# Optimization experiments

Measured on AMD Instinct MI355X. Metric: run time of the kernel, lower is better.

## Reference

```python
import jax, jax.numpy as jnp
import numpy as np

EPS = 1e-5

def _ln(x, g, b):
    m = jnp.mean(x, axis=-1, keepdims=True)
    v = jnp.mean((x - m) ** 2, axis=-1, keepdims=True)
    return (x - m) * jax.lax.rsqrt(v + EPS) * g + b


def setup_inputs() -> dict:
    key = jax.random.key(0)
    B, T, C, H, A = 4, 1024, 1024, 16, 64
    ks = jax.random.split(key, 16)
    s = 0.02
    inp = {
        "x": jax.random.normal(ks[0], (B, T, C), jnp.float32),
        "ln1_g": jnp.ones((C,), jnp.float32), "ln1_b": jnp.zeros((C,), jnp.float32),
        "ln2_g": jnp.ones((C,), jnp.float32), "ln2_b": jnp.zeros((C,), jnp.float32),
        "ln3_g": jnp.ones((C,), jnp.float32), "ln3_b": jnp.zeros((C,), jnp.float32),
        "wq": jax.random.normal(ks[1], (C, C), jnp.float32) * s, "bq": jnp.zeros((C,), jnp.float32),
        "wk": jax.random.normal(ks[2], (C, C), jnp.float32) * s, "bk": jnp.zeros((C,), jnp.float32),
        "wv": jax.random.normal(ks[3], (C, C), jnp.float32) * s, "bv": jnp.zeros((C,), jnp.float32),
        "wo": jax.random.normal(ks[4], (C, C), jnp.float32) * s, "bo": jnp.zeros((C,), jnp.float32),
        "w1": jax.random.normal(ks[5], (C, 4 * C), jnp.float32) * s, "b1": jnp.zeros((4 * C,), jnp.float32),
        "w2": jax.random.normal(ks[6], (4 * C, C), jnp.float32) * s, "b2": jnp.zeros((C,), jnp.float32),
        "wd": jax.random.normal(ks[7], (C, A), jnp.float32) * 1e-4, "bd": jnp.zeros((A,), jnp.float32),
        "wu": jax.random.normal(ks[8], (A, C), jnp.float32) * 1e-4, "bu": jnp.zeros((C,), jnp.float32),
    }
    return inp


def _block(x, ln1_g, ln1_b, ln2_g, ln2_b, ln3_g, ln3_b,
           wq, bq, wk, bk, wv, bv, wo, bo, w1, b1, w2, b2, wd, bd, wu, bu):
    B, T, C = x.shape
    H = 16
    D = C // H
    normed = _ln(x, ln3_g, ln3_b)  # ln3 of original input, used by adapter

    # --- causal self-attention on ln1(x) ---
    h = _ln(x, ln1_g, ln1_b)
    q = (h @ wq + bq).reshape(B, T, H, D)
    k = (h @ wk + bk).reshape(B, T, H, D)
    v = (h @ wv + bv).reshape(B, T, H, D)
    att = jnp.einsum('bqhd,bkhd->bhqk', q, k) * (1.0 / np.sqrt(D))
    causal = jnp.tril(jnp.ones((T, T), bool))
    att = jnp.where(causal, att, -jnp.inf)
    att = jax.nn.softmax(att, axis=-1)
    y = jnp.einsum('bhqk,bkhd->bqhd', att, v).reshape(B, T, C)
    attn_out = y @ wo + bo

    hidden = x + attn_out
    # --- MLP on ln2(hidden) ---
    m = _ln(hidden, ln2_g, ln2_b)
    mlp_out = jax.nn.gelu(m @ w1 + b1, approximate=False) @ w2 + b2
    forward_states = hidden + mlp_out

    # --- adapter on ln3(original x) ---
    a = jax.nn.relu(normed @ wd + bd) @ wu + bu

    # dropout is identity (p=0 / eval)
    return hidden + forward_states + a


def reference(x, ln1_g, ln1_b, ln2_g, ln2_b, ln3_g, ln3_b,
              wq, bq, wk, bk, wv, bv, wo, bo, w1, b1, w2, b2, wd, bd, wu, bu):
    return _block(x, ln1_g, ln1_b, ln2_g, ln2_b, ln3_g, ln3_b,
                  wq, bq, wk, bk, wv, bv, wo, bo, w1, b1, w2, b2, wd, bd, wu, bu)
```

## Files before the change

### kernel.cpp

```cpp
#include <hip/hip_runtime.h>

typedef unsigned short u16;
typedef __bf16 bf16x8 __attribute__((ext_vector_type(8)));
typedef u16    u16x8  __attribute__((ext_vector_type(8)));
typedef float  f32x4  __attribute__((ext_vector_type(4)));

__device__ __forceinline__ u16 f2bf(float f) {
    union { float f; unsigned u; } x{f};
    unsigned r = x.u + 0x7fffu + ((x.u >> 16) & 1u);
    return (u16)(r >> 16);
}

__device__ __forceinline__ f32x4 mfma16(bf16x8 a, bf16x8 b, f32x4 c) {
    return __builtin_amdgcn_mfma_f32_16x16x32_bf16(a, b, c, 0, 0, 0);
}

__device__ __forceinline__ void async_ld16(const void* g, void* l) {
    __builtin_amdgcn_global_load_lds(
        (const __attribute__((address_space(1))) unsigned int*)g,
        (__attribute__((address_space(3))) unsigned int*)l, 16, 0, 0);
}

__global__ void transpose_to_bf16(const float* __restrict__ in, u16* __restrict__ out,
                                  int K, int N) {
    __shared__ float tile[64][65];
    const int k0 = blockIdx.y * 64, n0 = blockIdx.x * 64;
    const int tid = threadIdx.x;
    const int rr = tid >> 4, cc = tid & 15;
#pragma unroll
    for (int it = 0; it < 4; ++it) {
        const int r = rr + it * 16;
        float4 v = *(const float4*)(in + (long)(k0 + r) * N + n0 + cc * 4);
        tile[r][cc * 4 + 0] = v.x; tile[r][cc * 4 + 1] = v.y;
        tile[r][cc * 4 + 2] = v.z; tile[r][cc * 4 + 3] = v.w;
    }
    __syncthreads();
#pragma unroll
    for (int it = 0; it < 4; ++it) {
        const int n = rr + it * 16;
        ushort4 o;
        o.x = f2bf(tile[cc * 4 + 0][n]);
        o.y = f2bf(tile[cc * 4 + 1][n]);
        o.z = f2bf(tile[cc * 4 + 2][n]);
        o.w = f2bf(tile[cc * 4 + 3][n]);
        *(ushort4*)(out + (long)(n0 + n) * K + k0 + cc * 4) = o;
    }
}

__global__ void concat_bias(const float* __restrict__ bq, const float* __restrict__ bk,
                            const float* __restrict__ bv, float* __restrict__ out) {
    int i = blockIdx.x * 256 + threadIdx.x;
    out[i] = i < 1024 ? bq[i] : (i < 2048 ? bk[i - 1024] : bv[i - 2048]);
}

__global__ void ln_dual_kernel(const float* __restrict__ x,
                               const float* __restrict__ g1, const float* __restrict__ b1,
                               const float* __restrict__ g3, const float* __restrict__ b3,
                               u16* __restrict__ out1, u16* __restrict__ out3) {
    const int row = blockIdx.x;
    const long base = (long)row * 1024;
    const int t = threadIdx.x;
    float4 v = ((const float4*)(x + base))[t];
    float s = v.x + v.y + v.z + v.w;
    float ss = v.x * v.x + v.y * v.y + v.z * v.z + v.w * v.w;
    for (int o = 32; o > 0; o >>= 1) { s += __shfl_down(s, o); ss += __shfl_down(ss, o); }
    __shared__ float red[8];
    if ((t & 63) == 0) { red[t >> 6] = s; red[(t >> 6) + 4] = ss; }
    __syncthreads();
    float sum = red[0] + red[1] + red[2] + red[3];
    float sq  = red[4] + red[5] + red[6] + red[7];
    const float mean = sum * (1.f / 1024.f);
    const float rstd = rsqrtf(sq * (1.f / 1024.f) - mean * mean + 1e-5f);
    float4 G1 = ((const float4*)g1)[t], B1 = ((const float4*)b1)[t];
    float4 G3 = ((const float4*)g3)[t], B3 = ((const float4*)b3)[t];
    float n0 = (v.x - mean) * rstd, n1 = (v.y - mean) * rstd;
    float n2 = (v.z - mean) * rstd, n3 = (v.w - mean) * rstd;
    ushort4 o1, o3;
    o1.x = f2bf(n0 * G1.x + B1.x); o1.y = f2bf(n1 * G1.y + B1.y);
    o1.z = f2bf(n2 * G1.z + B1.z); o1.w = f2bf(n3 * G1.w + B1.w);
    o3.x = f2bf(n0 * G3.x + B3.x); o3.y = f2bf(n1 * G3.y + B3.y);
    o3.z = f2bf(n2 * G3.z + B3.z); o3.w = f2bf(n3 * G3.w + B3.w);
    ((ushort4*)(out1 + base))[t] = o1;
    ((ushort4*)(out3 + base))[t] = o3;
}

__global__ void ln_single_kernel(const float* __restrict__ x,
                                 const float* __restrict__ g, const float* __restrict__ b,
                                 u16* __restrict__ out) {
    const int row = blockIdx.x;
    const long base = (long)row * 1024;
    const int t = threadIdx.x;
    float4 v = ((const float4*)(x + base))[t];
    float s = v.x + v.y + v.z + v.w;
    float ss = v.x * v.x + v.y * v.y + v.z * v.z + v.w * v.w;
    for (int o = 32; o > 0; o >>= 1) { s += __shfl_down(s, o); ss += __shfl_down(ss, o); }
    __shared__ float red[8];
    if ((t & 63) == 0) { red[t >> 6] = s; red[(t >> 6) + 4] = ss; }
    __syncthreads();
    float sum = red[0] + red[1] + red[2] + red[3];
    float sq  = red[4] + red[5] + red[6] + red[7];
    const float mean = sum * (1.f / 1024.f);
    const float rstd = rsqrtf(sq * (1.f / 1024.f) - mean * mean + 1e-5f);
    float4 G = ((const float4*)g)[t], B = ((const float4*)b)[t];
    ushort4 o;
    o.x = f2bf((v.x - mean) * rstd * G.x + B.x);
    o.y = f2bf((v.y - mean) * rstd * G.y + B.y);
    o.z = f2bf((v.z - mean) * rstd * G.z + B.z);
    o.w = f2bf((v.w - mean) * rstd * G.w + B.w);
    ((ushort4*)(out + base))[t] = o;
}

__global__ void transpose_v(const u16* __restrict__ qkv, u16* __restrict__ vT) {
    const int bh = blockIdx.z, b = bh >> 4, hh = bh & 15;
    const int t0 = blockIdx.x * 32, d0 = blockIdx.y * 32;
    __shared__ u16 tile[32][33];
    const u16* src = qkv + (long)(b * 1024) * 3072 + 2048 + hh * 64;
    for (int i = threadIdx.y; i < 32; i += 8)
        tile[i][threadIdx.x] = src[(long)(t0 + i) * 3072 + d0 + threadIdx.x];
    __syncthreads();
    u16* dst = vT + (long)bh * 64 * 1024;
    for (int i = threadIdx.y; i < 32; i += 8)
        dst[(long)(d0 + i) * 1024 + t0 + threadIdx.x] = tile[threadIdx.x][i];
}

template <int BN, typename Epi>
__global__ __launch_bounds__(256, 2)
void gemm_kernel(const u16* __restrict__ A, const u16* __restrict__ Bt,
                 int M, int N, int K, Epi epi) {
    constexpr int AE = 128 * 32;
    constexpr int BE = BN * 32;
    constexpr int MI = (BN == 128) ? 4 : 2;
    __shared__ u16 sm[4][AE + BE];
    const int tid = threadIdx.x;
    const int m0 = blockIdx.y * 128;
    const int n0 = blockIdx.x * BN;
    const int wid = tid >> 6, lane = tid & 63;
    const int lr = lane & 15, lh = lane >> 4;
    const int wm = (BN == 128) ? (wid >> 1) * 64 : wid * 32;
    const int wn = (BN == 128) ? (wid & 1) * 64 : 0;

    const int cr = lane >> 2, lq = lane & 3;
    const int ra0 = wid * 32 + cr, ra1 = ra0 + 16;
    const int qa0 = lq ^ (ra0 & 3) ^ ((ra0 >> 2) & 3);
    const int qa1 = lq ^ (ra1 & 3) ^ ((ra1 >> 2) & 3);
    const long aoff0 = (long)(m0 + ra0) * K + qa0 * 8;
    const long aoff1 = (long)(m0 + ra1) * K + qa1 * 8;
    const int la0 = wid * 1024, la1 = la0 + 512;

    long boff0, boff1 = 0;
    int lb0, lb1 = 0;
    if (BN == 128) {
        boff0 = (long)min(n0 + ra0, N - 1) * K + qa0 * 8;
        boff1 = (long)min(n0 + ra1, N - 1) * K + qa1 * 8;
        lb0 = AE + wid * 1024; lb1 = lb0 + 512;
    } else {
        const int rb = wid * 16 + cr;
        const int qb = lq ^ (rb & 3) ^ ((rb >> 2) & 3);
        boff0 = (long)min(n0 + rb, N - 1) * K + qb * 8;
        lb0 = AE + wid * 512;
    }

    const int qoff = ((lh ^ (lr & 3) ^ ((lr >> 2) & 3)) & 3) * 8;

    f32x4 acc[MI][4] = {};
    const int nk = K / 32;

    auto stage = [&](int kt) {
        const long ko = (long)kt * 32;
        u16* s = sm[kt & 3];
        async_ld16(A + aoff0 + ko, s + la0);
        async_ld16(A + aoff1 + ko, s + la1);
        async_ld16(Bt + boff0 + ko, s + lb0);
        if constexpr (BN == 128) async_ld16(Bt + boff1 + ko, s + lb1);
    };
    auto compute = [&](int kt) {
        const u16* sA = sm[kt & 3];
        const u16* sB = sA + AE;
        bf16x8 af[MI], bfr[4];
#pragma unroll
        for (int i = 0; i < MI; ++i)
            af[i] = *(const bf16x8*)(sA + (wm + i * 16 + lr) * 32 + qoff);
#pragma unroll
        for (int j = 0; j < 4; ++j)
            bfr[j] = *(const bf16x8*)(sB + (wn + j * 16 + lr) * 32 + qoff);
#pragma unroll
        for (int i = 0; i < MI; ++i)
#pragma unroll
            for (int j = 0; j < 4; ++j)
                acc[i][j] = mfma16(af[i], bfr[j], acc[i][j]);
    };

    stage(0);
    stage(1);
    __syncthreads();
    for (int kt = 0; kt < nk; kt += 2) {
        if (kt + 2 < nk) stage(kt + 2);
        if (kt + 3 < nk) stage(kt + 3);
        compute(kt);
        compute(kt + 1);
        __syncthreads();
    }

#pragma unroll
    for (int i = 0; i < MI; ++i)
#pragma unroll
        for (int j = 0; j < 4; ++j) {
            const int col = n0 + wn + j * 16 + lr;
            if (col < N) {
#pragma unroll
                for (int r = 0; r < 4; ++r) {
                    const int row = m0 + wm + i * 16 + lh * 4 + r;
                    epi(row, col, acc[i][j][r]);
                }
            }
        }
}

struct EpiBF16Bias {
    u16* out; const float* bias; int ldo;
    __device__ void operator()(int r, int c, float v) const {
        out[(long)r * ldo + c] = f2bf(v + bias[c]);
    }
};
struct EpiResid {
    float* hidden; const float* bias; const float* x;
    __device__ void operator()(int r, int c, float v) const {
        long i = (long)r * 1024 + c; hidden[i] = v + bias[c] + x[i];
    }
};
struct EpiGelu {
    u16* out; const float* bias;
    __device__ void operator()(int r, int c, float v) const {
        float x = v + bias[c];
        float g = 0.5f * x * (1.f + erff(x * 0.70710678118654752f));
        out[(long)r * 4096 + c] = f2bf(g);
    }
};
struct EpiReluBF16 {
    u16* out; const float* bias;
    __device__ void operator()(int r, int c, float v) const {
        out[(long)r * 64 + c] = f2bf(fmaxf(v + bias[c], 0.f));
    }
};
struct EpiAdapter {
    float* out; const float* bias; const float* hidden;
    __device__ void operator()(int r, int c, float v) const {
        long i = (long)r * 1024 + c; out[i] = 2.f * hidden[i] + v + bias[c];
    }
};
struct EpiAddOut {
    float* out; const float* bias;
    __device__ void operator()(int r, int c, float v) const {
        long i = (long)r * 1024 + c; out[i] += v + bias[c];
    }
};

__global__ __launch_bounds__(256, 2)
void attn_kernel(const u16* __restrict__ qkv, const u16* __restrict__ vT,
                 u16* __restrict__ y) {
    const int bh = blockIdx.x, b = bh >> 4, hh = bh & 15;
    const int q0 = blockIdx.y * 128;
    const int tid = threadIdx.x, wid = tid >> 6, lane = tid & 63;
    const int lr = lane & 15, lh = lane >> 4;
    const int qw = q0 + wid * 32;

    __shared__ u16 smK[64 * 72];
    __shared__ u16 smV[64 * 72];
    __shared__ u16 smP[4 * 32 * 72];
    u16* pw = smP + wid * (32 * 72);

    const u16* qbase = qkv + (long)(b * 1024) * 3072 + hh * 64;
    const u16* kbase = qbase + 1024;
    const u16* vbase = vT + (long)bh * 64 * 1024;

    bf16x8 a_q[2][2];
#pragma unroll
    for (int mt = 0; mt < 2; ++mt)
#pragma unroll
        for (int ks = 0; ks < 2; ++ks) {
            uint4 t = *(const uint4*)(qbase + (long)(qw + mt * 16 + lr) * 3072 + ks * 32 + lh * 8);
            a_q[mt][ks] = __builtin_bit_cast(bf16x8, t);
        }

    bf16x8 ones;
    { u16x8 t = {0x3F80, 0x3F80, 0x3F80, 0x3F80, 0x3F80, 0x3F80, 0x3F80, 0x3F80};
      ones = __builtin_bit_cast(bf16x8, t); }

    f32x4 o_acc[2][4] = {};
    f32x4 l_acc[2] = {};
    f32x4 m_run[2] = {{-1e30f, -1e30f, -1e30f, -1e30f}, {-1e30f, -1e30f, -1e30f, -1e30f}};

    const int ntiles = q0 / 64 + 2;
    const int ck = tid >> 3, cs = (tid & 7) * 8;
    const int ck2 = (tid + 256) >> 3, cs2 = ((tid + 256) & 7) * 8;
    for (int kt = 0; kt < ntiles; ++kt) {
        const int k0 = kt * 64;
        __syncthreads();
        {
            uint4 kv0 = *(const uint4*)(kbase + (long)(k0 + ck) * 3072 + cs);
            uint4 kv1 = *(const uint4*)(kbase + (long)(k0 + ck2) * 3072 + cs2);
            *(uint4*)(smK + ck * 72 + cs) = kv0;
            *(uint4*)(smK + ck2 * 72 + cs2) = kv1;
            uint4 vv0 = *(const uint4*)(vbase + (long)ck * 1024 + k0 + cs);
            uint4 vv1 = *(const uint4*)(vbase + (long)ck2 * 1024 + k0 + cs2);
            *(uint4*)(smV + ck * 72 + cs) = vv0;
            *(uint4*)(smV + ck2 * 72 + cs2) = vv1;
        }
        __syncthreads();
        if (k0 > qw + 31) continue;

        bf16x8 bK[4][2];
#pragma unroll
        for (int nt = 0; nt < 4; ++nt)
#pragma unroll
            for (int ks = 0; ks < 2; ++ks)
                bK[nt][ks] = *(const bf16x8*)(smK + (nt * 16 + lr) * 72 + ks * 32 + lh * 8);

        f32x4 s[2][4];
#pragma unroll
        for (int mt = 0; mt < 2; ++mt)
#pragma unroll
            for (int nt = 0; nt < 4; ++nt) {
                f32x4 z = {0.f, 0.f, 0.f, 0.f};
                z = mfma16(a_q[mt][0], bK[nt][0], z);
                z = mfma16(a_q[mt][1], bK[nt][1], z);
                s[mt][nt] = z;
            }
#pragma unroll
        for (int mt = 0; mt < 2; ++mt) {
            const int qb = qw + mt * 16 + lh * 4;
#pragma unroll
            for (int nt = 0; nt < 4; ++nt) {
                const int kkg = k0 + nt * 16 + lr;
#pragma unroll
                for (int r = 0; r < 4; ++r) {
                    float v = s[mt][nt][r] * 0.125f;
                    if (kkg > qb + r) v = -1e30f;
                    s[mt][nt][r] = v;
                }
            }
        }
#pragma unroll
        for (int mt = 0; mt < 2; ++mt) {
            f32x4 mx = s[mt][0];
#pragma unroll
            for (int nt = 1; nt < 4; ++nt)
#pragma unroll
                for (int r = 0; r < 4; ++r) mx[r] = fmaxf(mx[r], s[mt][nt][r]);
#pragma unroll
            for (int xm = 1; xm < 16; xm <<= 1)
#pragma unroll
                for (int r = 0; r < 4; ++r) mx[r] = fmaxf(mx[r], __shfl_xor(mx[r], xm));
            f32x4 mnew, alpha;
#pragma unroll
            for (int r = 0; r < 4; ++r) {
                mnew[r] = fmaxf(m_run[mt][r], mx[r]);
                alpha[r] = __expf(m_run[mt][r] - mnew[r]);
            }
            m_run[mt] = mnew;
            l_acc[mt] *= alpha;
#pragma unroll
            for (int dt = 0; dt < 4; ++dt) o_acc[mt][dt] *= alpha;
#pragma unroll
            for (int nt = 0; nt < 4; ++nt)
#pragma unroll
                for (int r = 0; r < 4; ++r)
                    s[mt][nt][r] = __expf(s[mt][nt][r] - mnew[r]);
#pragma unroll
            for (int nt = 0; nt < 4; ++nt)
#pragma unroll
                for (int r = 0; r < 4; ++r)
                    pw[(mt * 16 + lh * 4 + r) * 72 + nt * 16 + lr] = f2bf(s[mt][nt][r]);
        }
        bf16x8 vf[4][2];
#pragma unroll
        for (int dt = 0; dt < 4; ++dt)
#pragma unroll
            for (int ks = 0; ks < 2; ++ks)
                vf[dt][ks] = *(const bf16x8*)(smV + (dt * 16 + lr) * 72 + ks * 32 + lh * 8);
#pragma unroll
        for (int mt = 0; mt < 2; ++mt) {
            bf16x8 pf0 = *(const bf16x8*)(pw + (mt * 16 + lr) * 72 + lh * 8);
            bf16x8 pf1 = *(const bf16x8*)(pw + (mt * 16 + lr) * 72 + 32 + lh * 8);
            l_acc[mt] = mfma16(pf0, ones, l_acc[mt]);
            l_acc[mt] = mfma16(pf1, ones, l_acc[mt]);
#pragma unroll
            for (int dt = 0; dt < 4; ++dt) {
                o_acc[mt][dt] = mfma16(pf0, vf[dt][0], o_acc[mt][dt]);
                o_acc[mt][dt] = mfma16(pf1, vf[dt][1], o_acc[mt][dt]);
            }
        }
    }
#pragma unroll
    for (int mt = 0; mt < 2; ++mt) {
        f32x4 linv;
#pragma unroll
        for (int r = 0; r < 4; ++r) linv[r] = 1.f / l_acc[mt][r];
#pragma unroll
        for (int dt = 0; dt < 4; ++dt) {
#pragma unroll
            for (int r = 0; r < 4; ++r) {
                const int tok = b * 1024 + qw + mt * 16 + lh * 4 + r;
                y[(long)tok * 1024 + hh * 64 + dt * 16 + lr] = f2bf(o_acc[mt][dt][r] * linv[r]);
            }
        }
    }
}

extern "C" void kernel_launch(void* const* d_in, const int* in_sizes, int n_in,
                              void* d_out, int out_size, void* d_ws, size_t ws_size,
                              hipStream_t stream) {
    const float* x    = (const float*)d_in[0];
    const float* ln1g = (const float*)d_in[1];
    const float* ln1b = (const float*)d_in[2];
    const float* ln2g = (const float*)d_in[3];
    const float* ln2b = (const float*)d_in[4];
    const float* ln3g = (const float*)d_in[5];
    const float* ln3b = (const float*)d_in[6];
    const float* wq = (const float*)d_in[7];  const float* bq = (const float*)d_in[8];
    const float* wk = (const float*)d_in[9];  const float* bk = (const float*)d_in[10];
    const float* wv = (const float*)d_in[11]; const float* bv = (const float*)d_in[12];
    const float* wo = (const float*)d_in[13]; const float* bo = (const float*)d_in[14];
    const float* w1 = (const float*)d_in[15]; const float* b1 = (const float*)d_in[16];
    const float* w2 = (const float*)d_in[17]; const float* b2 = (const float*)d_in[18];
    const float* wd = (const float*)d_in[19]; const float* bd = (const float*)d_in[20];
    const float* wu = (const float*)d_in[21]; const float* bu = (const float*)d_in[22];
    float* out = (float*)d_out;

    char* base = (char*)d_ws;
    size_t off = 0;
    auto carve = [&](size_t bytes) -> char* {
        char* p = base + off; off += (bytes + 255) & ~(size_t)255; return p;
    };
    u16* qkv_wt = (u16*)carve(3072L * 1024 * 2);
    u16* wo_t   = (u16*)carve(1024L * 1024 * 2);
    u16* w1_t   = (u16*)carve(4096L * 1024 * 2);
    u16* w2_t   = (u16*)carve(1024L * 4096 * 2);
    u16* wd_t   = (u16*)carve(64L * 1024 * 2);
    u16* wu_t   = (u16*)carve(1024L * 64 * 2);
    float* bqkv = (float*)carve(3072L * 4);
    u16* hbuf   = (u16*)carve(4096L * 1024 * 2);
    u16* nrm    = (u16*)carve(4096L * 1024 * 2);
    u16* qkvb   = (u16*)carve(4096L * 3072 * 2);
    u16* vT     = (u16*)carve(64L * 64 * 1024 * 2);
    u16* ybuf   = (u16*)carve(4096L * 1024 * 2);
    float* hid  = (float*)carve(4096L * 1024 * 4);
    u16* mbuf   = (u16*)carve(4096L * 1024 * 2);
    u16* act    = (u16*)carve(4096L * 4096 * 2);
    u16* t1     = (u16*)carve(4096L * 64 * 2);

    transpose_to_bf16<<<dim3(16, 16), 256, 0, stream>>>(wq, qkv_wt, 1024, 1024);
    transpose_to_bf16<<<dim3(16, 16), 256, 0, stream>>>(wk, qkv_wt + 1024L * 1024, 1024, 1024);
    transpose_to_bf16<<<dim3(16, 16), 256, 0, stream>>>(wv, qkv_wt + 2048L * 1024, 1024, 1024);
    transpose_to_bf16<<<dim3(16, 16), 256, 0, stream>>>(wo, wo_t, 1024, 1024);
    transpose_to_bf16<<<dim3(64, 16), 256, 0, stream>>>(w1, w1_t, 1024, 4096);
    transpose_to_bf16<<<dim3(16, 64), 256, 0, stream>>>(w2, w2_t, 4096, 1024);
    transpose_to_bf16<<<dim3(1, 16), 256, 0, stream>>>(wd, wd_t, 1024, 64);
    transpose_to_bf16<<<dim3(16, 1), 256, 0, stream>>>(wu, wu_t, 64, 1024);
    concat_bias<<<12, 256, 0, stream>>>(bq, bk, bv, bqkv);

    ln_dual_kernel<<<4096, 256, 0, stream>>>(x, ln1g, ln1b, ln3g, ln3b, hbuf, nrm);

    gemm_kernel<128><<<dim3(24, 32), 256, 0, stream>>>(hbuf, qkv_wt, 4096, 3072, 1024,
                                                       EpiBF16Bias{qkvb, bqkv, 3072});
    transpose_v<<<dim3(32, 2, 64), dim3(32, 8), 0, stream>>>(qkvb, vT);
    attn_kernel<<<dim3(64, 8), 256, 0, stream>>>(qkvb, vT, ybuf);
    gemm_kernel<64><<<dim3(16, 32), 256, 0, stream>>>(ybuf, wo_t, 4096, 1024, 1024,
                                                      EpiResid{hid, bo, x});
    ln_single_kernel<<<4096, 256, 0, stream>>>(hid, ln2g, ln2b, mbuf);
    gemm_kernel<128><<<dim3(32, 32), 256, 0, stream>>>(mbuf, w1_t, 4096, 4096, 1024,
                                                       EpiGelu{act, b1});
    gemm_kernel<64><<<dim3(1, 32), 256, 0, stream>>>(nrm, wd_t, 4096, 64, 1024,
                                                     EpiReluBF16{t1, bd});
    gemm_kernel<64><<<dim3(16, 32), 256, 0, stream>>>(t1, wu_t, 4096, 1024, 64,
                                                      EpiAdapter{out, bu, hid});
    gemm_kernel<128><<<dim3(8, 32), 256, 0, stream>>>(act, w2_t, 4096, 1024, 4096,
                                                      EpiAddOut{out, b2});
}
```

Baseline: 430.0 us.

## Split-K the down-projection GEMM with atomics, triple-buffer GEMM LDS, batch weight transposes

The w2 GEMM is split along K into two halves on grid z, and results are accumulated into the output with float atomicAdd. Only the first split adds the bias. This doubles the block count for the 256-block launch so more of the CUs are busy. The GEMM pipeline drops from four to three LDS stages, processes one k-tile per iteration, and raises the occupancy hints in launch_bounds. The four 1024x1024 weight transposes are merged into a single launch. In exchange, atomics add contention and make the float summation order nondeterministic, and the shallower pipeline may hide less memory latency.

```diff
diff --git a/kernel.cpp b/kernel.cpp
--- a/kernel.cpp
+++ b/kernel.cpp
@@ -19,6 +19,38 @@
     __builtin_amdgcn_global_load_lds(
         (const __attribute__((address_space(1))) unsigned int*)g,
         (__attribute__((address_space(3))) unsigned int*)l, 16, 0, 0);
+}
+
+__global__ void transpose4_to_bf16(const float* __restrict__ s0, const float* __restrict__ s1,
+                                   const float* __restrict__ s2, const float* __restrict__ s3,
+                                   u16* __restrict__ d0, u16* __restrict__ d1,
+                                   u16* __restrict__ d2, u16* __restrict__ d3) {
+    const float* srcs[4] = {s0, s1, s2, s3};
+    u16* dsts[4] = {d0, d1, d2, d3};
+    const float* __restrict__ in = srcs[blockIdx.z];
+    u16* __restrict__ out = dsts[blockIdx.z];
+    __shared__ float tile[64][65];
+    const int k0 = blockIdx.y * 64, n0 = blockIdx.x * 64;
+    const int tid = threadIdx.x;
+    const int rr = tid >> 4, cc = tid & 15;
+#pragma unroll
+    for (int it = 0; it < 4; ++it) {
+        const int r = rr + it * 16;
+        float4 v = *(const float4*)(in + (long)(k0 + r) * 1024 + n0 + cc * 4);
+        tile[r][cc * 4 + 0] = v.x; tile[r][cc * 4 + 1] = v.y;
+        tile[r][cc * 4 + 2] = v.z; tile[r][cc * 4 + 3] = v.w;
+    }
+    __syncthreads();
+#pragma unroll
+    for (int it = 0; it < 4; ++it) {
+        const int n = rr + it * 16;
+        ushort4 o;
+        o.x = f2bf(tile[cc * 4 + 0][n]);
+        o.y = f2bf(tile[cc * 4 + 1][n]);
+        o.z = f2bf(tile[cc * 4 + 2][n]);
+        o.w = f2bf(tile[cc * 4 + 3][n]);
+        *(ushort4*)(out + (long)(n0 + n) * 1024 + k0 + cc * 4) = o;
+    }
 }
 
 __global__ void transpose_to_bf16(const float* __restrict__ in, u16* __restrict__ out,
@@ -124,16 +156,17 @@
 }
 
 template <int BN, typename Epi>
-__global__ __launch_bounds__(256, 2)
+__global__ __launch_bounds__(256, (BN == 128) ? 3 : 4)
 void gemm_kernel(const u16* __restrict__ A, const u16* __restrict__ Bt,
-                 int M, int N, int K, Epi epi) {
+                 int M, int N, int K, int ld, Epi epi) {
     constexpr int AE = 128 * 32;
     constexpr int BE = BN * 32;
     constexpr int MI = (BN == 128) ? 4 : 2;
-    __shared__ u16 sm[4][AE + BE];
+    __shared__ u16 sm[3][AE + BE];
     const int tid = threadIdx.x;
     const int m0 = blockIdx.y * 128;
     const int n0 = blockIdx.x * BN;
+    const int k0g = blockIdx.z * K;
     const int wid = tid >> 6, lane = tid & 63;
     const int lr = lane & 15, lh = lane >> 4;
     const int wm = (BN == 128) ? (wid >> 1) * 64 : wid * 32;
@@ -143,20 +176,20 @@
     const int ra0 = wid * 32 + cr, ra1 = ra0 + 16;
     const int qa0 = lq ^ (ra0 & 3) ^ ((ra0 >> 2) & 3);
     const int qa1 = lq ^ (ra1 & 3) ^ ((ra1 >> 2) & 3);
-    const long aoff0 = (long)(m0 + ra0) * K + qa0 * 8;
-    const long aoff1 = (long)(m0 + ra1) * K + qa1 * 8;
+    const long aoff0 = (long)(m0 + ra0) * ld + k0g + qa0 * 8;
+    const long aoff1 = (long)(m0 + ra1) * ld + k0g + qa1 * 8;
     const int la0 = wid * 1024, la1 = la0 + 512;
 
     long boff0, boff1 = 0;
     int lb0, lb1 = 0;
     if (BN == 128) {
-        boff0 = (long)min(n0 + ra0, N - 1) * K + qa0 * 8;
-        boff1 = (long)min(n0 + ra1, N - 1) * K + qa1 * 8;
+        boff0 = (long)min(n0 + ra0, N - 1) * ld + k0g + qa0 * 8;
+        boff1 = (long)min(n0 + ra1, N - 1) * ld + k0g + qa1 * 8;
         lb0 = AE + wid * 1024; lb1 = lb0 + 512;
     } else {
         const int rb = wid * 16 + cr;
         const int qb = lq ^ (rb & 3) ^ ((rb >> 2) & 3);
-        boff0 = (long)min(n0 + rb, N - 1) * K + qb * 8;
+        boff0 = (long)min(n0 + rb, N - 1) * ld + k0g + qb * 8;
         lb0 = AE + wid * 512;
     }
 
@@ -167,14 +200,14 @@
 
     auto stage = [&](int kt) {
         const long ko = (long)kt * 32;
-        u16* s = sm[kt & 3];
+        u16* s = sm[kt % 3];
         async_ld16(A + aoff0 + ko, s + la0);
         async_ld16(A + aoff1 + ko, s + la1);
         async_ld16(Bt + boff0 + ko, s + lb0);
         if constexpr (BN == 128) async_ld16(Bt + boff1 + ko, s + lb1);
     };
     auto compute = [&](int kt) {
-        const u16* sA = sm[kt & 3];
+        const u16* sA = sm[kt % 3];
         const u16* sB = sA + AE;
         bf16x8 af[MI], bfr[4];
 #pragma unroll
@@ -193,11 +226,9 @@
     stage(0);
     stage(1);
     __syncthreads();
-    for (int kt = 0; kt < nk; kt += 2) {
+    for (int kt = 0; kt < nk; ++kt) {
         if (kt + 2 < nk) stage(kt + 2);
-        if (kt + 3 < nk) stage(kt + 3);
         compute(kt);
-        compute(kt + 1);
         __syncthreads();
     }
 
@@ -248,10 +279,11 @@
         long i = (long)r * 1024 + c; out[i] = 2.f * hidden[i] + v + bias[c];
     }
 };
-struct EpiAddOut {
+struct EpiAtomicOut {
     float* out; const float* bias;
     __device__ void operator()(int r, int c, float v) const {
-        long i = (long)r * 1024 + c; out[i] += v + bias[c];
+        if (blockIdx.z == 0) v += bias[c];
+        atomicAdd(out + (long)r * 1024 + c, v);
     }
 };
 
@@ -449,10 +481,8 @@
     u16* act    = (u16*)carve(4096L * 4096 * 2);
     u16* t1     = (u16*)carve(4096L * 64 * 2);
 
-    transpose_to_bf16<<<dim3(16, 16), 256, 0, stream>>>(wq, qkv_wt, 1024, 1024);
-    transpose_to_bf16<<<dim3(16, 16), 256, 0, stream>>>(wk, qkv_wt + 1024L * 1024, 1024, 1024);
-    transpose_to_bf16<<<dim3(16, 16), 256, 0, stream>>>(wv, qkv_wt + 2048L * 1024, 1024, 1024);
-    transpose_to_bf16<<<dim3(16, 16), 256, 0, stream>>>(wo, wo_t, 1024, 1024);
+    transpose4_to_bf16<<<dim3(16, 16, 4), 256, 0, stream>>>(
+        wq, wk, wv, wo, qkv_wt, qkv_wt + 1024L * 1024, qkv_wt + 2048L * 1024, wo_t);
     transpose_to_bf16<<<dim3(64, 16), 256, 0, stream>>>(w1, w1_t, 1024, 4096);
     transpose_to_bf16<<<dim3(16, 64), 256, 0, stream>>>(w2, w2_t, 4096, 1024);
     transpose_to_bf16<<<dim3(1, 16), 256, 0, stream>>>(wd, wd_t, 1024, 64);
@@ -461,19 +491,19 @@
 
     ln_dual_kernel<<<4096, 256, 0, stream>>>(x, ln1g, ln1b, ln3g, ln3b, hbuf, nrm);
 
-    gemm_kernel<128><<<dim3(24, 32), 256, 0, stream>>>(hbuf, qkv_wt, 4096, 3072, 1024,
+    gemm_kernel<128><<<dim3(24, 32), 256, 0, stream>>>(hbuf, qkv_wt, 4096, 3072, 1024, 1024,
                                                        EpiBF16Bias{qkvb, bqkv, 3072});
     transpose_v<<<dim3(32, 2, 64), dim3(32, 8), 0, stream>>>(qkvb, vT);
     attn_kernel<<<dim3(64, 8), 256, 0, stream>>>(qkvb, vT, ybuf);
-    gemm_kernel<64><<<dim3(16, 32), 256, 0, stream>>>(ybuf, wo_t, 4096, 1024, 1024,
+    gemm_kernel<64><<<dim3(16, 32), 256, 0, stream>>>(ybuf, wo_t, 4096, 1024, 1024, 1024,
                                                       EpiResid{hid, bo, x});
     ln_single_kernel<<<4096, 256, 0, stream>>>(hid, ln2g, ln2b, mbuf);
-    gemm_kernel<128><<<dim3(32, 32), 256, 0, stream>>>(mbuf, w1_t, 4096, 4096, 1024,
+    gemm_kernel<128><<<dim3(32, 32), 256, 0, stream>>>(mbuf, w1_t, 4096, 4096, 1024, 1024,
                                                        EpiGelu{act, b1});
-    gemm_kernel<64><<<dim3(1, 32), 256, 0, stream>>>(nrm, wd_t, 4096, 64, 1024,
+    gemm_kernel<64><<<dim3(1, 32), 256, 0, stream>>>(nrm, wd_t, 4096, 64, 1024, 1024,
                                                      EpiReluBF16{t1, bd});
-    gemm_kernel<64><<<dim3(16, 32), 256, 0, stream>>>(t1, wu_t, 4096, 1024, 64,
+    gemm_kernel<64><<<dim3(16, 32), 256, 0, stream>>>(t1, wu_t, 4096, 1024, 64, 64,
                                                       EpiAdapter{out, bu, hid});
-    gemm_kernel<128><<<dim3(8, 32), 256, 0, stream>>>(act, w2_t, 4096, 1024, 4096,
-                                                      EpiAddOut{out, b2});
-}
+    gemm_kernel<128><<<dim3(8, 32, 2), 256, 0, stream>>>(act, w2_t, 4096, 1024, 2048, 4096,
+                                                         EpiAtomicOut{out, b2});
+}
```

After: 445.0 us. +3.5%, slower.
